# Optimization experiments

Hardware: AMD Instinct MI355X
Metric: run time of the kernel (lower is better)

## Reference

```python
import jax, jax.numpy as jnp
import numpy as np

EMBED = 256
B, S = 4, 4096

def _linear_params(key, d):
    k1, k2 = jax.random.split(key)
    lim = 1.0 / np.sqrt(d)
    W = jax.random.uniform(k1, (d, d), jnp.float32, -lim, lim)
    b = jax.random.uniform(k2, (d,), jnp.float32, -lim, lim)
    return W, b

def setup_inputs() -> dict:
    key = jax.random.key(0)
    ks = jax.random.split(key, 6)
    x = jax.random.normal(ks[0], (B, S, EMBED), jnp.float32)
    Wq, bq = _linear_params(ks[1], EMBED)
    Wk, bk = _linear_params(ks[2], EMBED)
    Wv, bv = _linear_params(ks[3], EMBED)
    Wl, bl = _linear_params(ks[4], EMBED)
    g1 = jnp.ones((EMBED,), jnp.float32); be1 = jnp.zeros((EMBED,), jnp.float32)
    g2 = jnp.ones((EMBED,), jnp.float32); be2 = jnp.zeros((EMBED,), jnp.float32)
    return {"x": x, "Wq": Wq, "bq": bq, "Wk": Wk, "bk": bk, "Wv": Wv, "bv": bv,
            "Wl": Wl, "bl": bl, "g1": g1, "be1": be1, "g2": g2, "be2": be2}

def _layernorm(x, g, b, eps=1e-5):
    mu = jnp.mean(x, axis=-1, keepdims=True)
    var = jnp.mean(jnp.square(x - mu), axis=-1, keepdims=True)
    return (x - mu) * jax.lax.rsqrt(var + eps) * g + b

def reference(x, Wq, bq, Wk, bk, Wv, bv, Wl, bl, g1, be1, g2, be2):
    d = x.shape[-1]
    q = jnp.einsum('bsd,ed->bse', x, Wq) + bq
    k = jnp.einsum('bsd,ed->bse', x, Wk) + bk
    v = jnp.einsum('bsd,ed->bse', x, Wv) + bv
    scores = jnp.einsum('bqd,bkd->bqk', q, k) / np.sqrt(d).astype(np.float32)
    attn = jax.nn.softmax(scores, axis=-1)
    out = jnp.einsum('bqk,bkd->bqd', attn, v)
    h = _layernorm(x + out, g1, be1)
    # NOTE: same linear applied twice (as in the original module)
    h = jnp.einsum('bsd,ed->bse', h, Wl) + bl
    h = jax.nn.relu(h)
    h = jnp.einsum('bsd,ed->bse', h, Wl) + bl
    return _layernorm(x + h, g2, be2)
```

## Files before the change

### kernel.cpp

```cpp
#include <hip/hip_runtime.h>

typedef unsigned short u16;
typedef float  f32x4 __attribute__((ext_vector_type(4)));
typedef short  s16x8 __attribute__((ext_vector_type(8)));
typedef unsigned short u16x4 __attribute__((ext_vector_type(4)));

#define NT 4194304

__device__ __forceinline__ u16 f2b(float f) {
    unsigned b = __float_as_uint(f);
    return (u16)((b + 0x7FFFu + ((b >> 16) & 1u)) >> 16);
}
__device__ __forceinline__ float b2f(u16 u) { return __uint_as_float(((unsigned)u) << 16); }

__device__ __forceinline__ s16x8 pack8(const float* p) {
    f32x4 lo = *(const f32x4*)p, hi = *(const f32x4*)(p + 4);
    union { s16x8 v; u16 u[8]; } pu;
#pragma unroll
    for (int e = 0; e < 4; ++e) { pu.u[e] = f2b(lo[e]); pu.u[4 + e] = f2b(hi[e]); }
    return pu.v;
}

__device__ __forceinline__ int perm64(int r) {
    return (r & 0x23) | (((r >> 2) & 3) << 3) | (((r >> 4) & 1) << 2);
}

__device__ __forceinline__ void gload16(const u16* g, u16* l) {
    __builtin_amdgcn_global_load_lds(
        (const __attribute__((address_space(1))) unsigned int*)g,
        (__attribute__((address_space(3))) unsigned int*)l,
        16, 0, 0);
}

__global__ __launch_bounds__(256) void gemm_kv(const float* __restrict__ x,
                                               const float* __restrict__ Wk, const float* __restrict__ Wv,
                                               const float* __restrict__ bk, const float* __restrict__ bv,
                                               u16* __restrict__ k, u16* __restrict__ vt) {
    const int tid = threadIdx.x;
    const int wid = tid >> 6, lane = tid & 63, g = lane >> 4, lq = lane & 15;
    const int m0 = blockIdx.x * 64, n0 = blockIdx.y * 64, z = blockIdx.z;
    const float* W = z ? Wv : Wk;
    const float* bias = z ? bv : bk;

    const float* arow = x + (size_t)(m0 + wid * 16 + lq) * 256;
    s16x8 af[8];
#pragma unroll
    for (int kk = 0; kk < 8; ++kk) af[kk] = pack8(arow + kk * 32 + g * 8);

    f32x4 acc[4];
#pragma unroll
    for (int nf = 0; nf < 4; ++nf) { acc[nf][0]=0.f; acc[nf][1]=0.f; acc[nf][2]=0.f; acc[nf][3]=0.f; }
#pragma unroll
    for (int kk = 0; kk < 8; ++kk) {
#pragma unroll
        for (int nf = 0; nf < 4; ++nf) {
            s16x8 b = pack8(W + (size_t)(n0 + nf * 16 + lq) * 256 + kk * 32 + g * 8);
            acc[nf] = __builtin_amdgcn_mfma_f32_16x16x32_bf16(af[kk], b, acc[nf], 0, 0, 0);
        }
    }

    __shared__ __align__(16) u16 c_lds[64 * 64];
#pragma unroll
    for (int nf = 0; nf < 4; ++nf) {
        float bb = bias[n0 + nf * 16 + lq];
#pragma unroll
        for (int j = 0; j < 4; ++j) {
            float v = acc[nf][j] + bb;
            if (!z) c_lds[(wid * 16 + (g << 2) + j) * 64 + nf * 16 + lq] = f2b(v);
            else    c_lds[(nf * 16 + lq) * 64 + wid * 16 + (g << 2) + j] = f2b(v);
        }
    }
    __syncthreads();
    if (!z) {
#pragma unroll
        for (int r = 0; r < 2; ++r) {
            int o = (r * 256 + tid) * 8, row = o >> 6, col = o & 63;
            *(s16x8*)(k + (size_t)(m0 + row) * 256 + n0 + col) = *(const s16x8*)(c_lds + row * 64 + col);
        }
    } else {
        int bidx = m0 >> 12, s0 = m0 & 4095;
#pragma unroll
        for (int r = 0; r < 2; ++r) {
            int o = (r * 256 + tid) * 8, drow = o >> 6, col = o & 63;
            *(s16x8*)(vt + (size_t)bidx * 1048576 + (size_t)(n0 + drow) * 4096 + s0 + col) =
                *(const s16x8*)(c_lds + drow * 64 + col);
        }
    }
}

__global__ __launch_bounds__(256) void flash5(const float* __restrict__ x, const float* __restrict__ Wq,
                                              const float* __restrict__ bq,
                                              const u16* __restrict__ K, const u16* __restrict__ VT,
                                              u16* __restrict__ Opart, float* __restrict__ ml) {
    __shared__ __align__(16) u16 smem[32768];
    const int tid = threadIdx.x;
    const int wid = tid >> 6, lane = tid & 63, g = lane >> 4, lqi = lane & 15;
    const int b = blockIdx.x >> 5, q0 = (blockIdx.x & 31) << 7;
    const int s = blockIdx.y, kvbase = s << 10;

    f32x4 acc[2][16];
#pragma unroll
    for (int qh = 0; qh < 2; ++qh)
#pragma unroll
        for (int nf = 0; nf < 16; ++nf) { acc[qh][nf][0]=0.f; acc[qh][nf][1]=0.f; acc[qh][nf][2]=0.f; acc[qh][nf][3]=0.f; }

    {
        s16x8 af[2][8];
#pragma unroll
        for (int qh = 0; qh < 2; ++qh) {
            const float* arow = x + (size_t)(b * 4096 + q0 + wid * 32 + qh * 16 + lqi) * 256;
#pragma unroll
            for (int kk = 0; kk < 8; ++kk) af[qh][kk] = pack8(arow + kk * 32 + g * 8);
        }
#pragma unroll
        for (int kk = 0; kk < 8; ++kk) {
#pragma unroll
            for (int nf = 0; nf < 16; ++nf) {
                s16x8 wb = pack8(Wq + (size_t)(nf * 16 + lqi) * 256 + kk * 32 + g * 8);
                acc[0][nf] = __builtin_amdgcn_mfma_f32_16x16x32_bf16(af[0][kk], wb, acc[0][nf], 0, 0, 0);
                acc[1][nf] = __builtin_amdgcn_mfma_f32_16x16x32_bf16(af[1][kk], wb, acc[1][nf], 0, 0, 0);
            }
        }
        const float scale = 0.0625f * 1.44269504f;
#pragma unroll
        for (int qh = 0; qh < 2; ++qh)
#pragma unroll
            for (int nf = 0; nf < 16; ++nf) {
                float bb = bq[nf * 16 + lqi];
#pragma unroll
                for (int j = 0; j < 4; ++j) {
                    int row = wid * 32 + qh * 16 + (g << 2) + j;
                    int col = nf * 16 + lqi;
                    int addr = row * 256 + (((col >> 3) ^ (row & 7)) << 3) + (col & 7);
                    smem[addr] = f2b((acc[qh][nf][j] + bb) * scale);
                }
            }
    }
    __syncthreads();
    s16x8 qf[2][8];
#pragma unroll
    for (int qh = 0; qh < 2; ++qh) {
        int row = wid * 32 + qh * 16 + lqi;
#pragma unroll
        for (int kk = 0; kk < 8; ++kk)
            qf[qh][kk] = *(const s16x8*)(smem + row * 256 + ((((kk << 2) | g) ^ (row & 7)) << 3));
    }
    __syncthreads();

#pragma unroll
    for (int qh = 0; qh < 2; ++qh)
#pragma unroll
        for (int nf = 0; nf < 16; ++nf) { acc[qh][nf][0]=0.f; acc[qh][nf][1]=0.f; acc[qh][nf][2]=0.f; acc[qh][nf][3]=0.f; }
    float mrun[2] = {-1e30f, -1e30f}, lrun[2] = {0.f, 0.f};

    const u16* kb_ = K + (size_t)b * 4096 * 256;
    const u16* vb_ = VT + (size_t)b * 256 * 4096;

    int koff[4], voff[4];
#pragma unroll
    for (int r = 0; r < 4; ++r) {
        int c = r * 256 + tid;
        int row = c >> 5, ch = c & 31;
        koff[r] = perm64(row) * 256 + ((ch ^ (row & 7)) << 3);
        int vrow = c >> 2, vch = c & 3;
        voff[r] = vrow * 4096 + ((vch ^ ((vrow >> 1) & 3)) << 3);
    }

    auto STAGE = [&](int bufsel, int t) {
        const u16* kt = kb_ + (size_t)(kvbase + (t << 5)) * 256;
        const u16* vt = vb_ + (kvbase + (t << 5));
        u16* kl = smem + bufsel * 16384;
        u16* vl = kl + 8192;
#pragma unroll
        for (int r = 0; r < 4; ++r) gload16(kt + koff[r], kl + (r * 256 + tid) * 8);
#pragma unroll
        for (int r = 0; r < 4; ++r) gload16(vt + voff[r], vl + (r * 256 + tid) * 8);
    };

    auto COMPUTE = [&](int bufsel) {
        const u16* kbuf = smem + bufsel * 16384;
        const u16* vbuf = kbuf + 8192;
        f32x4 st[2][2];
#pragma unroll
        for (int qh = 0; qh < 2; ++qh)
#pragma unroll
            for (int f = 0; f < 2; ++f) { st[qh][f][0]=0.f; st[qh][f][1]=0.f; st[qh][f][2]=0.f; st[qh][f][3]=0.f; }
        __builtin_amdgcn_s_setprio(1);
#pragma unroll
        for (int kk = 0; kk < 8; ++kk) {
#pragma unroll
            for (int f = 0; f < 2; ++f) {
                int row = f * 16 + lqi;
                s16x8 a = *(const s16x8*)(kbuf + ((row << 5) + (((kk << 2) + g) ^ (row & 7))) * 8);
                st[0][f] = __builtin_amdgcn_mfma_f32_16x16x32_bf16(a, qf[0][kk], st[0][f], 0, 0, 0);
                st[1][f] = __builtin_amdgcn_mfma_f32_16x16x32_bf16(a, qf[1][kk], st[1][f], 0, 0, 0);
            }
        }
        __builtin_amdgcn_s_setprio(0);
        s16x8 pa[2];
#pragma unroll
        for (int qh = 0; qh < 2; ++qh) {
            float rm = fmaxf(fmaxf(st[qh][0][0], st[qh][0][1]), fmaxf(st[qh][0][2], st[qh][0][3]));
            rm = fmaxf(rm, fmaxf(fmaxf(st[qh][1][0], st[qh][1][1]), fmaxf(st[qh][1][2], st[qh][1][3])));
            rm = fmaxf(rm, __shfl_xor(rm, 16));
            rm = fmaxf(rm, __shfl_xor(rm, 32));
            if (!__all(rm - mrun[qh] <= 8.f)) {
                float mnew = fmaxf(mrun[qh], rm);
                float alpha = exp2f(mrun[qh] - mnew);
#pragma unroll
                for (int j = 0; j < 4; ++j) {
                    float a4 = __shfl(alpha, (g << 2) + j);
#pragma unroll
                    for (int nf = 0; nf < 16; ++nf) acc[qh][nf][j] *= a4;
                }
                mrun[qh] = mnew;
                lrun[qh] *= alpha;
            }
            float ps = 0.f;
#pragma unroll
            for (int f = 0; f < 2; ++f)
#pragma unroll
                for (int j = 0; j < 4; ++j) { float e = exp2f(st[qh][f][j] - mrun[qh]); st[qh][f][j] = e; ps += e; }
            ps += __shfl_xor(ps, 16);
            ps += __shfl_xor(ps, 32);
            lrun[qh] += ps;
            union { s16x8 v; u16 u[8]; } pu;
#pragma unroll
            for (int j2 = 0; j2 < 4; ++j2) { pu.u[j2] = f2b(st[qh][0][j2]); pu.u[4+j2] = f2b(st[qh][1][j2]); }
            pa[qh] = pu.v;
        }
        __builtin_amdgcn_s_setprio(1);
#pragma unroll
        for (int nf = 0; nf < 16; ++nf) {
            int row = (nf << 4) + lqi;
            s16x8 bv = *(const s16x8*)(vbuf + ((row << 2) + (g ^ ((row >> 1) & 3))) * 8);
            acc[0][nf] = __builtin_amdgcn_mfma_f32_16x16x32_bf16(pa[0], bv, acc[0][nf], 0, 0, 0);
            acc[1][nf] = __builtin_amdgcn_mfma_f32_16x16x32_bf16(pa[1], bv, acc[1][nf], 0, 0, 0);
        }
        __builtin_amdgcn_s_setprio(0);
    };

    STAGE(0, 0);
    for (int t2 = 0; t2 < 32; t2 += 2) {
        __syncthreads();
        STAGE(1, t2 + 1);
        COMPUTE(0);
        __syncthreads();
        if (t2 + 2 < 32) STAGE(0, t2 + 2);
        COMPUTE(1);
    }

    __syncthreads();
    float linv[2][4];
#pragma unroll
    for (int qh = 0; qh < 2; ++qh)
#pragma unroll
        for (int j = 0; j < 4; ++j) linv[qh][j] = 1.0f / __shfl(lrun[qh], (g << 2) + j);
    u16* o_lds = smem;
#pragma unroll
    for (int qh = 0; qh < 2; ++qh)
#pragma unroll
        for (int nf = 0; nf < 16; ++nf)
#pragma unroll
            for (int j = 0; j < 4; ++j)
                o_lds[(wid * 32 + qh * 16 + (g << 2) + j) * 256 + (nf << 4) + lqi] = f2b(acc[qh][nf][j] * linv[qh][j]);
    __syncthreads();
    u16* orow = Opart + (size_t)s * NT + (size_t)(b * 4096 + q0) * 256;
#pragma unroll
    for (int r = 0; r < 16; ++r) {
        int o = (r * 256 + tid) * 8, row = o >> 8, col = o & 255;
        *(s16x8*)(orow + (size_t)row * 256 + col) = *(const s16x8*)(o_lds + row * 256 + col);
    }
    if (lane < 16) {
#pragma unroll
        for (int qh = 0; qh < 2; ++qh) {
            int grow = b * 4096 + q0 + wid * 32 + qh * 16 + lqi;
            ml[s * 32768 + grow]         = mrun[qh];
            ml[s * 32768 + 16384 + grow] = lrun[qh];
        }
    }
}

__global__ __launch_bounds__(256) void recomb_ln1(const u16* __restrict__ Opart, const float* __restrict__ ml,
                                                  const float* __restrict__ x, const float* __restrict__ gam,
                                                  const float* __restrict__ bet, u16* __restrict__ h) {
    const int row = blockIdx.x * 4 + (threadIdx.x >> 6);
    const int lane = threadIdx.x & 63;
    float m[4], l[4];
#pragma unroll
    for (int s = 0; s < 4; ++s) { m[s] = ml[s * 32768 + row]; l[s] = ml[s * 32768 + 16384 + row]; }
    float mm = fmaxf(fmaxf(m[0], m[1]), fmaxf(m[2], m[3]));
    float a[4], tot = 0.f;
#pragma unroll
    for (int s = 0; s < 4; ++s) { a[s] = l[s] * exp2f(m[s] - mm); tot += a[s]; }
    float rs = 1.0f / tot;
    float r[4] = {0.f, 0.f, 0.f, 0.f};
#pragma unroll
    for (int s = 0; s < 4; ++s) {
        float w = a[s] * rs;
        u16x4 v = *(const u16x4*)(Opart + (size_t)s * NT + (size_t)row * 256 + lane * 4);
#pragma unroll
        for (int i = 0; i < 4; ++i) r[i] += w * b2f(v[i]);
    }
    f32x4 xv = *(const f32x4*)(x + (size_t)row * 256 + lane * 4);
    float sv[4];
#pragma unroll
    for (int i = 0; i < 4; ++i) sv[i] = xv[i] + r[i];
    float sum = sv[0] + sv[1] + sv[2] + sv[3];
    float sq = sv[0]*sv[0] + sv[1]*sv[1] + sv[2]*sv[2] + sv[3]*sv[3];
#pragma unroll
    for (int d = 1; d < 64; d <<= 1) { sum += __shfl_xor(sum, d); sq += __shfl_xor(sq, d); }
    float mean = sum * (1.f / 256.f);
    float var = sq * (1.f / 256.f) - mean * mean;
    float rstd = rsqrtf(var + 1e-5f);
    f32x4 gv = *(const f32x4*)(gam + lane * 4);
    f32x4 bv = *(const f32x4*)(bet + lane * 4);
    u16x4 y;
#pragma unroll
    for (int i = 0; i < 4; ++i) y[i] = f2b((sv[i] - mean) * rstd * gv[i] + bv[i]);
    *(u16x4*)(h + (size_t)row * 256 + lane * 4) = y;
}

template<int RELU>
__global__ __launch_bounds__(256) void gemm_lin(const u16* __restrict__ A, const float* __restrict__ W,
                                                const float* __restrict__ bias, u16* __restrict__ Cd) {
    const int tid = threadIdx.x;
    const int wid = tid >> 6, lane = tid & 63, g = lane >> 4, lq = lane & 15;
    const int m0 = blockIdx.x * 64, n0 = blockIdx.y * 64;

    const u16* arow = A + (size_t)(m0 + wid * 16 + lq) * 256;
    f32x4 acc[4];
#pragma unroll
    for (int nf = 0; nf < 4; ++nf) { acc[nf][0]=0.f; acc[nf][1]=0.f; acc[nf][2]=0.f; acc[nf][3]=0.f; }
#pragma unroll
    for (int kk = 0; kk < 8; ++kk) {
        s16x8 a = *(const s16x8*)(arow + kk * 32 + g * 8);
#pragma unroll
        for (int nf = 0; nf < 4; ++nf) {
            s16x8 b = pack8(W + (size_t)(n0 + nf * 16 + lq) * 256 + kk * 32 + g * 8);
            acc[nf] = __builtin_amdgcn_mfma_f32_16x16x32_bf16(a, b, acc[nf], 0, 0, 0);
        }
    }
    __shared__ __align__(16) u16 c_lds[64 * 64];
#pragma unroll
    for (int nf = 0; nf < 4; ++nf) {
        float bb = bias[n0 + nf * 16 + lq];
#pragma unroll
        for (int j = 0; j < 4; ++j) {
            float v = acc[nf][j] + bb;
            if (RELU) v = fmaxf(v, 0.f);
            c_lds[(wid * 16 + (g << 2) + j) * 64 + nf * 16 + lq] = f2b(v);
        }
    }
    __syncthreads();
#pragma unroll
    for (int r = 0; r < 2; ++r) {
        int o = (r * 256 + tid) * 8, row = o >> 6, col = o & 63;
        *(s16x8*)(Cd + (size_t)(m0 + row) * 256 + n0 + col) = *(const s16x8*)(c_lds + row * 64 + col);
    }
}

__global__ __launch_bounds__(256) void ln2_k(const float* __restrict__ x, const u16* __restrict__ add,
                                             const float* __restrict__ gam, const float* __restrict__ bet,
                                             float* __restrict__ outf) {
    const int row = blockIdx.x * 4 + (threadIdx.x >> 6);
    const int lane = threadIdx.x & 63;
    f32x4 xv = *(const f32x4*)(x + (size_t)row * 256 + lane * 4);
    u16x4 av = *(const u16x4*)(add + (size_t)row * 256 + lane * 4);
    float sv[4];
#pragma unroll
    for (int i = 0; i < 4; ++i) sv[i] = xv[i] + b2f(av[i]);
    float sum = sv[0] + sv[1] + sv[2] + sv[3];
    float sq = sv[0]*sv[0] + sv[1]*sv[1] + sv[2]*sv[2] + sv[3]*sv[3];
#pragma unroll
    for (int d = 1; d < 64; d <<= 1) { sum += __shfl_xor(sum, d); sq += __shfl_xor(sq, d); }
    float mean = sum * (1.f / 256.f);
    float var = sq * (1.f / 256.f) - mean * mean;
    float rstd = rsqrtf(var + 1e-5f);
    f32x4 gv = *(const f32x4*)(gam + lane * 4);
    f32x4 bv = *(const f32x4*)(bet + lane * 4);
    f32x4 y;
#pragma unroll
    for (int i = 0; i < 4; ++i) y[i] = (sv[i] - mean) * rstd * gv[i] + bv[i];
    *(f32x4*)(outf + (size_t)row * 256 + lane * 4) = y;
}

extern "C" void kernel_launch(void* const* d_in, const int* in_sizes, int n_in,
                              void* d_out, int out_size, void* d_ws, size_t ws_size,
                              hipStream_t stream) {
    const float* x   = (const float*)d_in[0];
    const float* Wq  = (const float*)d_in[1];
    const float* bq  = (const float*)d_in[2];
    const float* Wk  = (const float*)d_in[3];
    const float* bk  = (const float*)d_in[4];
    const float* Wv  = (const float*)d_in[5];
    const float* bv  = (const float*)d_in[6];
    const float* Wl  = (const float*)d_in[7];
    const float* bl  = (const float*)d_in[8];
    const float* g1  = (const float*)d_in[9];
    const float* be1 = (const float*)d_in[10];
    const float* g2  = (const float*)d_in[11];
    const float* be2 = (const float*)d_in[12];
    float* out = (float*)d_out;

    u16* kb   = (u16*)d_ws;
    u16* vtb  = kb + NT;
    u16* op   = vtb + NT;
    float* ml = (float*)(op + (size_t)4 * NT);

    gemm_kv<<<dim3(256, 4, 2), 256, 0, stream>>>(x, Wk, Wv, bk, bv, kb, vtb);

    flash5<<<dim3(128, 4), 256, 0, stream>>>(x, Wq, bq, kb, vtb, op, ml);

    recomb_ln1<<<4096, 256, 0, stream>>>(op, ml, x, g1, be1, kb );

    dim3 ggrid(256, 4);
    gemm_lin<1><<<ggrid, 256, 0, stream>>>(kb, Wl, bl, vtb );
    gemm_lin<0><<<ggrid, 256, 0, stream>>>(vtb, Wl, bl, op );

    ln2_k<<<4096, 256, 0, stream>>>(x, op, g2, be2, out);
}
```

Baseline: 443.7 us.

## Pre-convert weights to bf16, retile flash attention, fuse tail into one kernel

Adds a one-shot kernel that converts all four weight matrices to bf16, so the GEMMs load packed bf16 instead of converting fp32 on every load. The flash kernel now handles 64 query rows per block (one 16-row tile per wave) over 2 KV splits of 2048 keys, where before it handled 128 rows over 4 splits. Split recombination, LN1, both Wl linears with ReLU, and LN2 are fused into a single kernel that keeps intermediates in LDS, removing four launches and the global round trips between them. The trade-off is less MFMA reuse per Q fragment, a longer serial KV loop per block, and a tail kernel with only 256 blocks.

```diff
diff --git a/kernel.cpp b/kernel.cpp
--- a/kernel.cpp
+++ b/kernel.cpp
@@ -32,14 +32,26 @@
         16, 0, 0);
 }
 
-__global__ __launch_bounds__(256) void gemm_kv(const float* __restrict__ x,
-                                               const float* __restrict__ Wk, const float* __restrict__ Wv,
+__global__ __launch_bounds__(256) void cvt_w4(const float* __restrict__ w0, const float* __restrict__ w1,
+                                              const float* __restrict__ w2, const float* __restrict__ w3,
+                                              u16* __restrict__ dst) {
+    const int z = blockIdx.y;
+    const float* src = z == 0 ? w0 : z == 1 ? w1 : z == 2 ? w2 : w3;
+    int i = (blockIdx.x * 256 + threadIdx.x) * 4;
+    f32x4 v = *(const f32x4*)(src + i);
+    u16x4 o;
+    o[0] = f2b(v[0]); o[1] = f2b(v[1]); o[2] = f2b(v[2]); o[3] = f2b(v[3]);
+    *(u16x4*)(dst + (size_t)z * 65536 + i) = o;
+}
+
+__global__ __launch_bounds__(256) void gemm_kv(const float* __restrict__ x, const u16* __restrict__ wk,
+                                               const u16* __restrict__ wv,
                                                const float* __restrict__ bk, const float* __restrict__ bv,
                                                u16* __restrict__ k, u16* __restrict__ vt) {
     const int tid = threadIdx.x;
     const int wid = tid >> 6, lane = tid & 63, g = lane >> 4, lq = lane & 15;
     const int m0 = blockIdx.x * 64, n0 = blockIdx.y * 64, z = blockIdx.z;
-    const float* W = z ? Wv : Wk;
+    const u16* W = z ? wv : wk;
     const float* bias = z ? bv : bk;
 
     const float* arow = x + (size_t)(m0 + wid * 16 + lq) * 256;
@@ -54,7 +66,7 @@
     for (int kk = 0; kk < 8; ++kk) {
 #pragma unroll
         for (int nf = 0; nf < 4; ++nf) {
-            s16x8 b = pack8(W + (size_t)(n0 + nf * 16 + lq) * 256 + kk * 32 + g * 8);
+            s16x8 b = *(const s16x8*)(W + (size_t)(n0 + nf * 16 + lq) * 256 + kk * 32 + g * 8);
             acc[nf] = __builtin_amdgcn_mfma_f32_16x16x32_bf16(af[kk], b, acc[nf], 0, 0, 0);
         }
     }
@@ -88,70 +100,58 @@
     }
 }
 
-__global__ __launch_bounds__(256) void flash5(const float* __restrict__ x, const float* __restrict__ Wq,
+__global__ __launch_bounds__(256) void flash6(const float* __restrict__ x, const u16* __restrict__ wq,
                                               const float* __restrict__ bq,
                                               const u16* __restrict__ K, const u16* __restrict__ VT,
                                               u16* __restrict__ Opart, float* __restrict__ ml) {
     __shared__ __align__(16) u16 smem[32768];
     const int tid = threadIdx.x;
     const int wid = tid >> 6, lane = tid & 63, g = lane >> 4, lqi = lane & 15;
-    const int b = blockIdx.x >> 5, q0 = (blockIdx.x & 31) << 7;
-    const int s = blockIdx.y, kvbase = s << 10;
-
-    f32x4 acc[2][16];
-#pragma unroll
-    for (int qh = 0; qh < 2; ++qh)
-#pragma unroll
-        for (int nf = 0; nf < 16; ++nf) { acc[qh][nf][0]=0.f; acc[qh][nf][1]=0.f; acc[qh][nf][2]=0.f; acc[qh][nf][3]=0.f; }
+    const int b = blockIdx.x >> 6, q0 = (blockIdx.x & 63) << 6;
+    const int s = blockIdx.y, kvbase = s << 11;
+
+    f32x4 acc[16];
+#pragma unroll
+    for (int nf = 0; nf < 16; ++nf) { acc[nf][0]=0.f; acc[nf][1]=0.f; acc[nf][2]=0.f; acc[nf][3]=0.f; }
 
     {
-        s16x8 af[2][8];
-#pragma unroll
-        for (int qh = 0; qh < 2; ++qh) {
-            const float* arow = x + (size_t)(b * 4096 + q0 + wid * 32 + qh * 16 + lqi) * 256;
-#pragma unroll
-            for (int kk = 0; kk < 8; ++kk) af[qh][kk] = pack8(arow + kk * 32 + g * 8);
-        }
-#pragma unroll
-        for (int kk = 0; kk < 8; ++kk) {
+        const float* arow = x + (size_t)(b * 4096 + q0 + wid * 16 + lqi) * 256;
+        s16x8 af[8];
+#pragma unroll
+        for (int kk = 0; kk < 8; ++kk) af[kk] = pack8(arow + kk * 32 + g * 8);
+#pragma unroll
+        for (int kk = 0; kk < 8; ++kk)
 #pragma unroll
             for (int nf = 0; nf < 16; ++nf) {
-                s16x8 wb = pack8(Wq + (size_t)(nf * 16 + lqi) * 256 + kk * 32 + g * 8);
-                acc[0][nf] = __builtin_amdgcn_mfma_f32_16x16x32_bf16(af[0][kk], wb, acc[0][nf], 0, 0, 0);
-                acc[1][nf] = __builtin_amdgcn_mfma_f32_16x16x32_bf16(af[1][kk], wb, acc[1][nf], 0, 0, 0);
-            }
-        }
+                s16x8 wb = *(const s16x8*)(wq + (size_t)(nf * 16 + lqi) * 256 + kk * 32 + g * 8);
+                acc[nf] = __builtin_amdgcn_mfma_f32_16x16x32_bf16(af[kk], wb, acc[nf], 0, 0, 0);
+            }
         const float scale = 0.0625f * 1.44269504f;
 #pragma unroll
-        for (int qh = 0; qh < 2; ++qh)
-#pragma unroll
-            for (int nf = 0; nf < 16; ++nf) {
-                float bb = bq[nf * 16 + lqi];
-#pragma unroll
-                for (int j = 0; j < 4; ++j) {
-                    int row = wid * 32 + qh * 16 + (g << 2) + j;
-                    int col = nf * 16 + lqi;
-                    int addr = row * 256 + (((col >> 3) ^ (row & 7)) << 3) + (col & 7);
-                    smem[addr] = f2b((acc[qh][nf][j] + bb) * scale);
-                }
-            }
-    }
-    __syncthreads();
-    s16x8 qf[2][8];
-#pragma unroll
-    for (int qh = 0; qh < 2; ++qh) {
-        int row = wid * 32 + qh * 16 + lqi;
+        for (int nf = 0; nf < 16; ++nf) {
+            float bb = bq[nf * 16 + lqi];
+#pragma unroll
+            for (int j = 0; j < 4; ++j) {
+                int row = wid * 16 + (g << 2) + j;
+                int col = nf * 16 + lqi;
+                int addr = row * 256 + (((col >> 3) ^ (row & 7)) << 3) + (col & 7);
+                smem[addr] = f2b((acc[nf][j] + bb) * scale);
+            }
+        }
+    }
+    __syncthreads();
+    s16x8 qf[8];
+    {
+        int row = wid * 16 + lqi;
 #pragma unroll
         for (int kk = 0; kk < 8; ++kk)
-            qf[qh][kk] = *(const s16x8*)(smem + row * 256 + ((((kk << 2) | g) ^ (row & 7)) << 3));
-    }
-    __syncthreads();
-
-#pragma unroll
-    for (int qh = 0; qh < 2; ++qh)
-#pragma unroll
-        for (int nf = 0; nf < 16; ++nf) { acc[qh][nf][0]=0.f; acc[qh][nf][1]=0.f; acc[qh][nf][2]=0.f; acc[qh][nf][3]=0.f; }
-    float mrun[2] = {-1e30f, -1e30f}, lrun[2] = {0.f, 0.f};
+            qf[kk] = *(const s16x8*)(smem + row * 256 + ((((kk << 2) | g) ^ (row & 7)) << 3));
+    }
+    __syncthreads();
+
+#pragma unroll
+    for (int nf = 0; nf < 16; ++nf) { acc[nf][0]=0.f; acc[nf][1]=0.f; acc[nf][2]=0.f; acc[nf][3]=0.f; }
+    float mrun = -1e30f, lrun = 0.f;
 
     const u16* kb_ = K + (size_t)b * 4096 * 256;
     const u16* vb_ = VT + (size_t)b * 256 * 4096;
@@ -180,11 +180,9 @@
     auto COMPUTE = [&](int bufsel) {
         const u16* kbuf = smem + bufsel * 16384;
         const u16* vbuf = kbuf + 8192;
-        f32x4 st[2][2];
-#pragma unroll
-        for (int qh = 0; qh < 2; ++qh)
-#pragma unroll
-            for (int f = 0; f < 2; ++f) { st[qh][f][0]=0.f; st[qh][f][1]=0.f; st[qh][f][2]=0.f; st[qh][f][3]=0.f; }
+        f32x4 st[2];
+#pragma unroll
+        for (int f = 0; f < 2; ++f) { st[f][0]=0.f; st[f][1]=0.f; st[f][2]=0.f; st[f][3]=0.f; }
         __builtin_amdgcn_s_setprio(1);
 #pragma unroll
         for (int kk = 0; kk < 8; ++kk) {
@@ -192,197 +190,205 @@
             for (int f = 0; f < 2; ++f) {
                 int row = f * 16 + lqi;
                 s16x8 a = *(const s16x8*)(kbuf + ((row << 5) + (((kk << 2) + g) ^ (row & 7))) * 8);
-                st[0][f] = __builtin_amdgcn_mfma_f32_16x16x32_bf16(a, qf[0][kk], st[0][f], 0, 0, 0);
-                st[1][f] = __builtin_amdgcn_mfma_f32_16x16x32_bf16(a, qf[1][kk], st[1][f], 0, 0, 0);
+                st[f] = __builtin_amdgcn_mfma_f32_16x16x32_bf16(a, qf[kk], st[f], 0, 0, 0);
             }
         }
         __builtin_amdgcn_s_setprio(0);
-        s16x8 pa[2];
-#pragma unroll
-        for (int qh = 0; qh < 2; ++qh) {
-            float rm = fmaxf(fmaxf(st[qh][0][0], st[qh][0][1]), fmaxf(st[qh][0][2], st[qh][0][3]));
-            rm = fmaxf(rm, fmaxf(fmaxf(st[qh][1][0], st[qh][1][1]), fmaxf(st[qh][1][2], st[qh][1][3])));
-            rm = fmaxf(rm, __shfl_xor(rm, 16));
-            rm = fmaxf(rm, __shfl_xor(rm, 32));
-            if (!__all(rm - mrun[qh] <= 8.f)) {
-                float mnew = fmaxf(mrun[qh], rm);
-                float alpha = exp2f(mrun[qh] - mnew);
-#pragma unroll
-                for (int j = 0; j < 4; ++j) {
-                    float a4 = __shfl(alpha, (g << 2) + j);
-#pragma unroll
-                    for (int nf = 0; nf < 16; ++nf) acc[qh][nf][j] *= a4;
-                }
-                mrun[qh] = mnew;
-                lrun[qh] *= alpha;
-            }
-            float ps = 0.f;
-#pragma unroll
-            for (int f = 0; f < 2; ++f)
-#pragma unroll
-                for (int j = 0; j < 4; ++j) { float e = exp2f(st[qh][f][j] - mrun[qh]); st[qh][f][j] = e; ps += e; }
-            ps += __shfl_xor(ps, 16);
-            ps += __shfl_xor(ps, 32);
-            lrun[qh] += ps;
+        float rm = fmaxf(fmaxf(st[0][0], st[0][1]), fmaxf(st[0][2], st[0][3]));
+        rm = fmaxf(rm, fmaxf(fmaxf(st[1][0], st[1][1]), fmaxf(st[1][2], st[1][3])));
+        rm = fmaxf(rm, __shfl_xor(rm, 16));
+        rm = fmaxf(rm, __shfl_xor(rm, 32));
+        if (!__all(rm - mrun <= 8.f)) {
+            float mnew = fmaxf(mrun, rm);
+            float alpha = exp2f(mrun - mnew);
+#pragma unroll
+            for (int j = 0; j < 4; ++j) {
+                float a4 = __shfl(alpha, (g << 2) + j);
+#pragma unroll
+                for (int nf = 0; nf < 16; ++nf) acc[nf][j] *= a4;
+            }
+            mrun = mnew;
+            lrun *= alpha;
+        }
+        float ps = 0.f;
+#pragma unroll
+        for (int f = 0; f < 2; ++f)
+#pragma unroll
+            for (int j = 0; j < 4; ++j) { float e = exp2f(st[f][j] - mrun); st[f][j] = e; ps += e; }
+        ps += __shfl_xor(ps, 16);
+        ps += __shfl_xor(ps, 32);
+        lrun += ps;
+        s16x8 pa;
+        {
             union { s16x8 v; u16 u[8]; } pu;
 #pragma unroll
-            for (int j2 = 0; j2 < 4; ++j2) { pu.u[j2] = f2b(st[qh][0][j2]); pu.u[4+j2] = f2b(st[qh][1][j2]); }
-            pa[qh] = pu.v;
+            for (int j2 = 0; j2 < 4; ++j2) { pu.u[j2] = f2b(st[0][j2]); pu.u[4+j2] = f2b(st[1][j2]); }
+            pa = pu.v;
         }
         __builtin_amdgcn_s_setprio(1);
 #pragma unroll
         for (int nf = 0; nf < 16; ++nf) {
             int row = (nf << 4) + lqi;
             s16x8 bv = *(const s16x8*)(vbuf + ((row << 2) + (g ^ ((row >> 1) & 3))) * 8);
-            acc[0][nf] = __builtin_amdgcn_mfma_f32_16x16x32_bf16(pa[0], bv, acc[0][nf], 0, 0, 0);
-            acc[1][nf] = __builtin_amdgcn_mfma_f32_16x16x32_bf16(pa[1], bv, acc[1][nf], 0, 0, 0);
+            acc[nf] = __builtin_amdgcn_mfma_f32_16x16x32_bf16(pa, bv, acc[nf], 0, 0, 0);
         }
         __builtin_amdgcn_s_setprio(0);
     };
 
     STAGE(0, 0);
-    for (int t2 = 0; t2 < 32; t2 += 2) {
+    for (int t2 = 0; t2 < 64; t2 += 2) {
         __syncthreads();
         STAGE(1, t2 + 1);
         COMPUTE(0);
         __syncthreads();
-        if (t2 + 2 < 32) STAGE(0, t2 + 2);
+        if (t2 + 2 < 64) STAGE(0, t2 + 2);
         COMPUTE(1);
     }
 
     __syncthreads();
-    float linv[2][4];
-#pragma unroll
-    for (int qh = 0; qh < 2; ++qh)
-#pragma unroll
-        for (int j = 0; j < 4; ++j) linv[qh][j] = 1.0f / __shfl(lrun[qh], (g << 2) + j);
+    float linv[4];
+#pragma unroll
+    for (int j = 0; j < 4; ++j) linv[j] = 1.0f / __shfl(lrun, (g << 2) + j);
     u16* o_lds = smem;
 #pragma unroll
-    for (int qh = 0; qh < 2; ++qh)
-#pragma unroll
-        for (int nf = 0; nf < 16; ++nf)
-#pragma unroll
-            for (int j = 0; j < 4; ++j)
-                o_lds[(wid * 32 + qh * 16 + (g << 2) + j) * 256 + (nf << 4) + lqi] = f2b(acc[qh][nf][j] * linv[qh][j]);
+    for (int nf = 0; nf < 16; ++nf)
+#pragma unroll
+        for (int j = 0; j < 4; ++j)
+            o_lds[(wid * 16 + (g << 2) + j) * 256 + (nf << 4) + lqi] = f2b(acc[nf][j] * linv[j]);
     __syncthreads();
     u16* orow = Opart + (size_t)s * NT + (size_t)(b * 4096 + q0) * 256;
 #pragma unroll
-    for (int r = 0; r < 16; ++r) {
+    for (int r = 0; r < 8; ++r) {
         int o = (r * 256 + tid) * 8, row = o >> 8, col = o & 255;
         *(s16x8*)(orow + (size_t)row * 256 + col) = *(const s16x8*)(o_lds + row * 256 + col);
     }
     if (lane < 16) {
-#pragma unroll
-        for (int qh = 0; qh < 2; ++qh) {
-            int grow = b * 4096 + q0 + wid * 32 + qh * 16 + lqi;
-            ml[s * 32768 + grow]         = mrun[qh];
-            ml[s * 32768 + 16384 + grow] = lrun[qh];
-        }
-    }
-}
-
-__global__ __launch_bounds__(256) void recomb_ln1(const u16* __restrict__ Opart, const float* __restrict__ ml,
-                                                  const float* __restrict__ x, const float* __restrict__ gam,
-                                                  const float* __restrict__ bet, u16* __restrict__ h) {
-    const int row = blockIdx.x * 4 + (threadIdx.x >> 6);
-    const int lane = threadIdx.x & 63;
-    float m[4], l[4];
-#pragma unroll
-    for (int s = 0; s < 4; ++s) { m[s] = ml[s * 32768 + row]; l[s] = ml[s * 32768 + 16384 + row]; }
-    float mm = fmaxf(fmaxf(m[0], m[1]), fmaxf(m[2], m[3]));
-    float a[4], tot = 0.f;
-#pragma unroll
-    for (int s = 0; s < 4; ++s) { a[s] = l[s] * exp2f(m[s] - mm); tot += a[s]; }
-    float rs = 1.0f / tot;
-    float r[4] = {0.f, 0.f, 0.f, 0.f};
-#pragma unroll
-    for (int s = 0; s < 4; ++s) {
-        float w = a[s] * rs;
-        u16x4 v = *(const u16x4*)(Opart + (size_t)s * NT + (size_t)row * 256 + lane * 4);
-#pragma unroll
-        for (int i = 0; i < 4; ++i) r[i] += w * b2f(v[i]);
-    }
-    f32x4 xv = *(const f32x4*)(x + (size_t)row * 256 + lane * 4);
-    float sv[4];
-#pragma unroll
-    for (int i = 0; i < 4; ++i) sv[i] = xv[i] + r[i];
-    float sum = sv[0] + sv[1] + sv[2] + sv[3];
-    float sq = sv[0]*sv[0] + sv[1]*sv[1] + sv[2]*sv[2] + sv[3]*sv[3];
-#pragma unroll
-    for (int d = 1; d < 64; d <<= 1) { sum += __shfl_xor(sum, d); sq += __shfl_xor(sq, d); }
-    float mean = sum * (1.f / 256.f);
-    float var = sq * (1.f / 256.f) - mean * mean;
-    float rstd = rsqrtf(var + 1e-5f);
-    f32x4 gv = *(const f32x4*)(gam + lane * 4);
-    f32x4 bv = *(const f32x4*)(bet + lane * 4);
-    u16x4 y;
-#pragma unroll
-    for (int i = 0; i < 4; ++i) y[i] = f2b((sv[i] - mean) * rstd * gv[i] + bv[i]);
-    *(u16x4*)(h + (size_t)row * 256 + lane * 4) = y;
-}
-
-template<int RELU>
-__global__ __launch_bounds__(256) void gemm_lin(const u16* __restrict__ A, const float* __restrict__ W,
-                                                const float* __restrict__ bias, u16* __restrict__ Cd) {
+        int grow = b * 4096 + q0 + wid * 16 + lqi;
+        ml[s * 32768 + grow]         = mrun;
+        ml[s * 32768 + 16384 + grow] = lrun;
+    }
+}
+
+__global__ __launch_bounds__(256) void tail_fused(const u16* __restrict__ Opart, const float* __restrict__ ml,
+                                                  const float* __restrict__ x,
+                                                  const float* __restrict__ g1, const float* __restrict__ be1,
+                                                  const u16* __restrict__ wl, const float* __restrict__ bl,
+                                                  const float* __restrict__ g2, const float* __restrict__ be2,
+                                                  float* __restrict__ out) {
+    __shared__ __align__(16) u16 smem[32768];
+    u16* bufA = smem;
+    u16* bufB = smem + 16384;
     const int tid = threadIdx.x;
-    const int wid = tid >> 6, lane = tid & 63, g = lane >> 4, lq = lane & 15;
-    const int m0 = blockIdx.x * 64, n0 = blockIdx.y * 64;
-
-    const u16* arow = A + (size_t)(m0 + wid * 16 + lq) * 256;
-    f32x4 acc[4];
-#pragma unroll
-    for (int nf = 0; nf < 4; ++nf) { acc[nf][0]=0.f; acc[nf][1]=0.f; acc[nf][2]=0.f; acc[nf][3]=0.f; }
-#pragma unroll
-    for (int kk = 0; kk < 8; ++kk) {
-        s16x8 a = *(const s16x8*)(arow + kk * 32 + g * 8);
-#pragma unroll
-        for (int nf = 0; nf < 4; ++nf) {
-            s16x8 b = pack8(W + (size_t)(n0 + nf * 16 + lq) * 256 + kk * 32 + g * 8);
-            acc[nf] = __builtin_amdgcn_mfma_f32_16x16x32_bf16(a, b, acc[nf], 0, 0, 0);
-        }
-    }
-    __shared__ __align__(16) u16 c_lds[64 * 64];
-#pragma unroll
-    for (int nf = 0; nf < 4; ++nf) {
-        float bb = bias[n0 + nf * 16 + lq];
-#pragma unroll
-        for (int j = 0; j < 4; ++j) {
-            float v = acc[nf][j] + bb;
-            if (RELU) v = fmaxf(v, 0.f);
-            c_lds[(wid * 16 + (g << 2) + j) * 64 + nf * 16 + lq] = f2b(v);
-        }
-    }
-    __syncthreads();
-#pragma unroll
-    for (int r = 0; r < 2; ++r) {
-        int o = (r * 256 + tid) * 8, row = o >> 6, col = o & 63;
-        *(s16x8*)(Cd + (size_t)(m0 + row) * 256 + n0 + col) = *(const s16x8*)(c_lds + row * 64 + col);
-    }
-}
-
-__global__ __launch_bounds__(256) void ln2_k(const float* __restrict__ x, const u16* __restrict__ add,
-                                             const float* __restrict__ gam, const float* __restrict__ bet,
-                                             float* __restrict__ outf) {
-    const int row = blockIdx.x * 4 + (threadIdx.x >> 6);
-    const int lane = threadIdx.x & 63;
-    f32x4 xv = *(const f32x4*)(x + (size_t)row * 256 + lane * 4);
-    u16x4 av = *(const u16x4*)(add + (size_t)row * 256 + lane * 4);
-    float sv[4];
-#pragma unroll
-    for (int i = 0; i < 4; ++i) sv[i] = xv[i] + b2f(av[i]);
-    float sum = sv[0] + sv[1] + sv[2] + sv[3];
-    float sq = sv[0]*sv[0] + sv[1]*sv[1] + sv[2]*sv[2] + sv[3]*sv[3];
-#pragma unroll
-    for (int d = 1; d < 64; d <<= 1) { sum += __shfl_xor(sum, d); sq += __shfl_xor(sq, d); }
-    float mean = sum * (1.f / 256.f);
-    float var = sq * (1.f / 256.f) - mean * mean;
-    float rstd = rsqrtf(var + 1e-5f);
-    f32x4 gv = *(const f32x4*)(gam + lane * 4);
-    f32x4 bv = *(const f32x4*)(bet + lane * 4);
-    f32x4 y;
-#pragma unroll
-    for (int i = 0; i < 4; ++i) y[i] = (sv[i] - mean) * rstd * gv[i] + bv[i];
-    *(f32x4*)(outf + (size_t)row * 256 + lane * 4) = y;
+    const int wid = tid >> 6, lane = tid & 63, g = lane >> 4, lqi = lane & 15;
+    const int m0 = blockIdx.x * 64;
+
+#pragma unroll 1
+    for (int r = 0; r < 16; ++r) {
+        int rl = wid * 16 + r;
+        int row = m0 + rl;
+        float m0v = ml[row],         l0 = ml[16384 + row];
+        float m1v = ml[32768 + row], l1 = ml[49152 + row];
+        float mm = fmaxf(m0v, m1v);
+        float a0 = l0 * exp2f(m0v - mm), a1 = l1 * exp2f(m1v - mm);
+        float rs = 1.0f / (a0 + a1);
+        a0 *= rs; a1 *= rs;
+        u16x4 v0 = *(const u16x4*)(Opart + (size_t)row * 256 + lane * 4);
+        u16x4 v1 = *(const u16x4*)(Opart + NT + (size_t)row * 256 + lane * 4);
+        f32x4 xv = *(const f32x4*)(x + (size_t)row * 256 + lane * 4);
+        float sv[4];
+#pragma unroll
+        for (int i = 0; i < 4; ++i) sv[i] = xv[i] + a0 * b2f(v0[i]) + a1 * b2f(v1[i]);
+        float sum = sv[0]+sv[1]+sv[2]+sv[3];
+        float sq = sv[0]*sv[0]+sv[1]*sv[1]+sv[2]*sv[2]+sv[3]*sv[3];
+#pragma unroll
+        for (int d = 1; d < 64; d <<= 1) { sum += __shfl_xor(sum, d); sq += __shfl_xor(sq, d); }
+        float mean = sum * (1.f/256.f);
+        float rstd = rsqrtf(sq * (1.f/256.f) - mean*mean + 1e-5f);
+        int c = lane * 4;
+        int addr = rl * 256 + ((((c >> 3) ^ (rl & 7)) << 3)) + (c & 7);
+        u16x4 y;
+#pragma unroll
+        for (int i = 0; i < 4; ++i) y[i] = f2b((sv[i] - mean) * rstd * g1[c + i] + be1[c + i]);
+        *(u16x4*)(bufA + addr) = y;
+    }
+    __syncthreads();
+
+    {
+        f32x4 acc[16];
+#pragma unroll
+        for (int nf = 0; nf < 16; ++nf) { acc[nf][0]=0.f; acc[nf][1]=0.f; acc[nf][2]=0.f; acc[nf][3]=0.f; }
+        int rl = wid * 16 + lqi;
+#pragma unroll
+        for (int kk = 0; kk < 8; ++kk) {
+            s16x8 a = *(const s16x8*)(bufA + rl * 256 + ((((kk << 2) | g) ^ (rl & 7)) << 3));
+#pragma unroll
+            for (int nf = 0; nf < 16; ++nf) {
+                s16x8 b = *(const s16x8*)(wl + (size_t)(nf * 16 + lqi) * 256 + kk * 32 + g * 8);
+                acc[nf] = __builtin_amdgcn_mfma_f32_16x16x32_bf16(a, b, acc[nf], 0, 0, 0);
+            }
+        }
+        __syncthreads();
+#pragma unroll
+        for (int nf = 0; nf < 16; ++nf) {
+            float bb = bl[nf * 16 + lqi];
+            int c = nf * 16 + lqi, ch = c >> 3, lo = c & 7;
+#pragma unroll
+            for (int j = 0; j < 4; ++j) {
+                int ml_ = wid * 16 + (g << 2) + j;
+                bufB[ml_ * 256 + (((ch ^ (ml_ & 7)) << 3)) + lo] = f2b(fmaxf(acc[nf][j] + bb, 0.f));
+            }
+        }
+    }
+    __syncthreads();
+
+    {
+        f32x4 acc[16];
+#pragma unroll
+        for (int nf = 0; nf < 16; ++nf) { acc[nf][0]=0.f; acc[nf][1]=0.f; acc[nf][2]=0.f; acc[nf][3]=0.f; }
+        int rl = wid * 16 + lqi;
+#pragma unroll
+        for (int kk = 0; kk < 8; ++kk) {
+            s16x8 a = *(const s16x8*)(bufB + rl * 256 + ((((kk << 2) | g) ^ (rl & 7)) << 3));
+#pragma unroll
+            for (int nf = 0; nf < 16; ++nf) {
+                s16x8 b = *(const s16x8*)(wl + (size_t)(nf * 16 + lqi) * 256 + kk * 32 + g * 8);
+                acc[nf] = __builtin_amdgcn_mfma_f32_16x16x32_bf16(a, b, acc[nf], 0, 0, 0);
+            }
+        }
+        __syncthreads();
+#pragma unroll
+        for (int nf = 0; nf < 16; ++nf) {
+            float bb = bl[nf * 16 + lqi];
+#pragma unroll
+            for (int j = 0; j < 4; ++j) {
+                int ml_ = wid * 16 + (g << 2) + j;
+                bufA[ml_ * 256 + nf * 16 + lqi] = f2b(acc[nf][j] + bb);
+            }
+        }
+    }
+    __syncthreads();
+
+#pragma unroll 1
+    for (int r = 0; r < 16; ++r) {
+        int rl = wid * 16 + r;
+        int row = m0 + rl;
+        u16x4 av = *(const u16x4*)(bufA + rl * 256 + lane * 4);
+        f32x4 xv = *(const f32x4*)(x + (size_t)row * 256 + lane * 4);
+        float sv[4];
+#pragma unroll
+        for (int i = 0; i < 4; ++i) sv[i] = xv[i] + b2f(av[i]);
+        float sum = sv[0]+sv[1]+sv[2]+sv[3];
+        float sq = sv[0]*sv[0]+sv[1]*sv[1]+sv[2]*sv[2]+sv[3]*sv[3];
+#pragma unroll
+        for (int d = 1; d < 64; d <<= 1) { sum += __shfl_xor(sum, d); sq += __shfl_xor(sq, d); }
+        float mean = sum * (1.f/256.f);
+        float rstd = rsqrtf(sq * (1.f/256.f) - mean*mean + 1e-5f);
+        int c = lane * 4;
+        f32x4 y;
+#pragma unroll
+        for (int i = 0; i < 4; ++i) y[i] = (sv[i] - mean) * rstd * g2[c + i] + be2[c + i];
+        *(f32x4*)(out + (size_t)row * 256 + c) = y;
+    }
 }
 
 extern "C" void kernel_launch(void* const* d_in, const int* in_sizes, int n_in,
@@ -403,20 +409,20 @@
     const float* be2 = (const float*)d_in[12];
     float* out = (float*)d_out;
 
-    u16* kb   = (u16*)d_ws;
+    u16* wqb  = (u16*)d_ws;
+    u16* wkb  = wqb + 65536;
+    u16* wvb  = wkb + 65536;
+    u16* wlb  = wvb + 65536;
+    u16* kb   = wlb + 65536;
     u16* vtb  = kb + NT;
     u16* op   = vtb + NT;
-    float* ml = (float*)(op + (size_t)4 * NT);
-
-    gemm_kv<<<dim3(256, 4, 2), 256, 0, stream>>>(x, Wk, Wv, bk, bv, kb, vtb);
-
-    flash5<<<dim3(128, 4), 256, 0, stream>>>(x, Wq, bq, kb, vtb, op, ml);
-
-    recomb_ln1<<<4096, 256, 0, stream>>>(op, ml, x, g1, be1, kb );
-
-    dim3 ggrid(256, 4);
-    gemm_lin<1><<<ggrid, 256, 0, stream>>>(kb, Wl, bl, vtb );
-    gemm_lin<0><<<ggrid, 256, 0, stream>>>(vtb, Wl, bl, op );
-
-    ln2_k<<<4096, 256, 0, stream>>>(x, op, g2, be2, out);
-}
+    float* ml = (float*)(op + (size_t)2 * NT);
+
+    cvt_w4<<<dim3(64, 4), 256, 0, stream>>>(Wq, Wk, Wv, Wl, wqb);
+
+    gemm_kv<<<dim3(256, 4, 2), 256, 0, stream>>>(x, wkb, wvb, bk, bv, kb, vtb);
+
+    flash6<<<dim3(256, 2), 256, 0, stream>>>(x, wqb, bq, kb, vtb, op, ml);
+
+    tail_fused<<<256, 256, 0, stream>>>(op, ml, x, g1, be1, wlb, bl, g2, be2, out);
+}
```

After: 390.0 us. 1.14x faster.
